# Optimization experiments

Measured on AMD Instinct MI355X. Metric: run time of the kernel, lower is better.

Reference implementation:

```python
import jax, jax.numpy as jnp
import numpy as np

V, H, B, T = 100000, 512, 4096, 524288
EPS = 1e-5

def setup_inputs() -> dict:
    key = jax.random.key(0)
    ks = jax.random.split(key, 8)
    tokens = jax.random.randint(ks[0], (T,), 0, V, dtype=jnp.int32)
    seg_ids = jnp.sort(jax.random.randint(ks[1], (T,), 0, B, dtype=jnp.int32))
    t = jax.random.bernoulli(ks[2], 0.5, (B,)).astype(jnp.float32)
    emb = jax.random.normal(ks[3], (V, H), dtype=jnp.float32) * 0.1
    W1 = jax.random.normal(ks[4], (H, H), dtype=jnp.float32) * (1.0 / np.sqrt(H))
    b1 = jnp.zeros((H,), jnp.float32)
    gamma = jnp.ones((H,), jnp.float32)
    beta = jnp.zeros((H,), jnp.float32)
    w2 = jax.random.normal(ks[5], (H,), dtype=jnp.float32) * (1.0 / np.sqrt(H))
    b2 = jnp.zeros((), jnp.float32)
    return {"tokens": tokens, "seg_ids": seg_ids, "t": t, "emb": emb,
            "W1": W1, "b1": b1, "gamma": gamma, "beta": beta, "w2": w2, "b2": b2}

def reference(tokens, seg_ids, t, emb, W1, b1, gamma, beta, w2, b2):
    nb = t.shape[0]
    # fused gather + segment-mean (bag-of-words), replaces the per-sample loop
    gathered = emb[tokens]  # [T, H]
    sums = jax.ops.segment_sum(gathered, seg_ids, num_segments=nb)  # [B, H]
    counts = jax.ops.segment_sum(jnp.ones((tokens.shape[0],), jnp.float32), seg_ids, num_segments=nb)
    bow = sums / jnp.maximum(counts, 1.0)[:, None]  # [B, H]
    # Linear -> BatchNorm1d (training-mode batch stats, biased var) -> ReLU
    z = bow @ W1.T + b1  # [B, H]
    mu = jnp.mean(z, axis=0)
    var = jnp.mean((z - mu) ** 2, axis=0)
    zn = (z - mu) * jax.lax.rsqrt(var + EPS) * gamma + beta
    h = jax.nn.relu(zn)  # dropout treated as identity (eval mode) for determinism
    logits = h @ w2 + b2  # [B]
    # BCEWithLogitsLoss: mean(softplus(logit) - t*logit), numerically stable
    loss = jnp.mean(jnp.logaddexp(0.0, logits) - t * logits)
    return (loss, logits)
```

## Files before the change

### kernel.cpp

```cpp
#include <hip/hip_runtime.h>
#include <hip/hip_bf16.h>
#include <math.h>

constexpr int NTOK = 524288;
constexpr int NB   = 4096;
constexpr int H    = 512;
constexpr float EPS = 1e-5f;

__global__ __launch_bounds__(128) void k_gather_mean(
    const int* __restrict__ tokens, const int* __restrict__ seg,
    const float* __restrict__ emb, float* __restrict__ bow) {
  const int b = blockIdx.x;
  int lo = 0, hi = NTOK;
  while (lo < hi) { int mid = (lo + hi) >> 1; if (seg[mid] < b) lo = mid + 1; else hi = mid; }
  const int start = lo;
  hi = NTOK;
  while (lo < hi) { int mid = (lo + hi) >> 1; if (seg[mid] < b + 1) lo = mid + 1; else hi = mid; }
  const int end = lo;

  const int tid = threadIdx.x;
  const float4* __restrict__ emb4 = (const float4*)emb;
  float4 acc = make_float4(0.f, 0.f, 0.f, 0.f);

  int i = start;
  for (; i + 4 <= end; i += 4) {
    int t0 = tokens[i], t1 = tokens[i + 1], t2 = tokens[i + 2], t3 = tokens[i + 3];
    float4 v0 = emb4[(size_t)t0 * 128 + tid];
    float4 v1 = emb4[(size_t)t1 * 128 + tid];
    float4 v2 = emb4[(size_t)t2 * 128 + tid];
    float4 v3 = emb4[(size_t)t3 * 128 + tid];
    acc.x += v0.x + v1.x + v2.x + v3.x;
    acc.y += v0.y + v1.y + v2.y + v3.y;
    acc.z += v0.z + v1.z + v2.z + v3.z;
    acc.w += v0.w + v1.w + v2.w + v3.w;
  }
  for (; i < end; ++i) {
    int t0 = tokens[i];
    float4 v0 = emb4[(size_t)t0 * 128 + tid];
    acc.x += v0.x; acc.y += v0.y; acc.z += v0.z; acc.w += v0.w;
  }
  const int cnt = end - start;
  const float s = 1.0f / (float)(cnt > 0 ? cnt : 1);
  acc.x *= s; acc.y *= s; acc.z *= s; acc.w *= s;
  ((float4*)bow)[(size_t)b * 128 + tid] = acc;
}

constexpr int BM = 64, BN = 64, BK = 32;
constexpr int LST = BM + 4;

__global__ __launch_bounds__(256) void k_gemm(
    const float* __restrict__ A, const float* __restrict__ W,
    const float* __restrict__ b1, float* __restrict__ C) {
  __shared__ float As[BK][LST];
  __shared__ float Bs[BK][LST];
  const int tid = threadIdx.x;
  const int tx = tid & 15, ty = tid >> 4;
  const int bm0 = blockIdx.x * BM;
  const int bn0 = blockIdx.y * BN;

  const int lrow = tid >> 3;
  const int lc4  = (tid & 7) * 4;

  float acc[4][4] = {};

  for (int kc = 0; kc < H; kc += BK) {
    float4 a0 = *(const float4*)&A[(size_t)(bm0 + lrow)      * H + kc + lc4];
    float4 a1 = *(const float4*)&A[(size_t)(bm0 + lrow + 32) * H + kc + lc4];
    float4 w0 = *(const float4*)&W[(size_t)(bn0 + lrow)      * H + kc + lc4];
    float4 w1 = *(const float4*)&W[(size_t)(bn0 + lrow + 32) * H + kc + lc4];
    __syncthreads();
    As[lc4 + 0][lrow] = a0.x; As[lc4 + 1][lrow] = a0.y;
    As[lc4 + 2][lrow] = a0.z; As[lc4 + 3][lrow] = a0.w;
    As[lc4 + 0][lrow + 32] = a1.x; As[lc4 + 1][lrow + 32] = a1.y;
    As[lc4 + 2][lrow + 32] = a1.z; As[lc4 + 3][lrow + 32] = a1.w;
    Bs[lc4 + 0][lrow] = w0.x; Bs[lc4 + 1][lrow] = w0.y;
    Bs[lc4 + 2][lrow] = w0.z; Bs[lc4 + 3][lrow] = w0.w;
    Bs[lc4 + 0][lrow + 32] = w1.x; Bs[lc4 + 1][lrow + 32] = w1.y;
    Bs[lc4 + 2][lrow + 32] = w1.z; Bs[lc4 + 3][lrow + 32] = w1.w;
    __syncthreads();
#pragma unroll
    for (int k = 0; k < BK; ++k) {
      float4 av = *(const float4*)&As[k][ty * 4];
      float4 bv = *(const float4*)&Bs[k][tx * 4];
      acc[0][0] += av.x * bv.x; acc[0][1] += av.x * bv.y; acc[0][2] += av.x * bv.z; acc[0][3] += av.x * bv.w;
      acc[1][0] += av.y * bv.x; acc[1][1] += av.y * bv.y; acc[1][2] += av.y * bv.z; acc[1][3] += av.y * bv.w;
      acc[2][0] += av.z * bv.x; acc[2][1] += av.z * bv.y; acc[2][2] += av.z * bv.z; acc[2][3] += av.z * bv.w;
      acc[3][0] += av.w * bv.x; acc[3][1] += av.w * bv.y; acc[3][2] += av.w * bv.z; acc[3][3] += av.w * bv.w;
    }
  }
  const float4 bb = *(const float4*)&b1[bn0 + tx * 4];
#pragma unroll
  for (int i = 0; i < 4; ++i) {
    float4 o;
    o.x = acc[i][0] + bb.x; o.y = acc[i][1] + bb.y;
    o.z = acc[i][2] + bb.z; o.w = acc[i][3] + bb.w;
    *(float4*)&C[(size_t)(bm0 + ty * 4 + i) * H + bn0 + tx * 4] = o;
  }
}

__global__ __launch_bounds__(256) void k_colstats(
    const float* __restrict__ z, float* __restrict__ ps, float* __restrict__ pss) {
  const int blk = blockIdx.x;
  const int c0 = threadIdx.x * 2;
  const int r0 = blk * 64;
  float s0 = 0, s1 = 0, q0 = 0, q1 = 0;
  for (int r = 0; r < 64; ++r) {
    float2 v = *(const float2*)&z[(size_t)(r0 + r) * H + c0];
    s0 += v.x; s1 += v.y;
    q0 += v.x * v.x; q1 += v.y * v.y;
  }
  ps[blk * H + c0] = s0; ps[blk * H + c0 + 1] = s1;
  pss[blk * H + c0] = q0; pss[blk * H + c0 + 1] = q1;
}

__global__ __launch_bounds__(512) void k_finalize(
    const float* __restrict__ ps, const float* __restrict__ pss,
    const float* __restrict__ gamma, const float* __restrict__ beta,
    float* __restrict__ scale, float* __restrict__ shift) {
  const int c = threadIdx.x;
  float s = 0, q = 0;
  for (int i = 0; i < 64; ++i) { s += ps[i * H + c]; q += pss[i * H + c]; }
  const float mu = s * (1.0f / NB);
  const float var = q * (1.0f / NB) - mu * mu;
  const float rstd = rsqrtf(var + EPS);
  const float sc = rstd * gamma[c];
  scale[c] = sc;
  shift[c] = beta[c] - mu * sc;
}

__global__ __launch_bounds__(256) void k_bn_dot(
    const float* __restrict__ z, const float* __restrict__ scale,
    const float* __restrict__ shift, const float* __restrict__ w2,
    const float* __restrict__ b2, float* __restrict__ out) {
  const int tid = threadIdx.x;
  const int wave = tid >> 6, lane = tid & 63;
  const int b = blockIdx.x * 4 + wave;
  const float4* __restrict__ z4 = (const float4*)(z + (size_t)b * H);
  const float4* __restrict__ sc4 = (const float4*)scale;
  const float4* __restrict__ sh4 = (const float4*)shift;
  const float4* __restrict__ w24 = (const float4*)w2;
  float acc = 0.f;
#pragma unroll
  for (int i = lane; i < 128; i += 64) {
    float4 zv = z4[i], sc = sc4[i], sh = sh4[i], w = w24[i];
    float h0 = fmaxf(zv.x * sc.x + sh.x, 0.f);
    float h1 = fmaxf(zv.y * sc.y + sh.y, 0.f);
    float h2 = fmaxf(zv.z * sc.z + sh.z, 0.f);
    float h3 = fmaxf(zv.w * sc.w + sh.w, 0.f);
    acc += h0 * w.x + h1 * w.y + h2 * w.z + h3 * w.w;
  }
#pragma unroll
  for (int off = 32; off > 0; off >>= 1) acc += __shfl_down(acc, off, 64);
  if (lane == 0) out[1 + b] = acc + b2[0];
}

__global__ __launch_bounds__(256) void k_loss(
    const float* __restrict__ t, float* __restrict__ d_out) {
  const int tid = threadIdx.x;
  float s = 0.f;
  for (int b = tid; b < NB; b += 256) {
    float x = d_out[1 + b];
    float sp = fmaxf(x, 0.f) + log1pf(expf(-fabsf(x)));
    s += sp - t[b] * x;
  }
  __shared__ float red[256];
  red[tid] = s;
  __syncthreads();
  for (int off = 128; off > 0; off >>= 1) {
    if (tid < off) red[tid] += red[tid + off];
    __syncthreads();
  }
  if (tid == 0) d_out[0] = red[0] * (1.0f / NB);
}

extern "C" void kernel_launch(void* const* d_in, const int* in_sizes, int n_in,
                              void* d_out, int out_size, void* d_ws, size_t ws_size,
                              hipStream_t stream) {
  const int*   tokens = (const int*)d_in[0];
  const int*   seg    = (const int*)d_in[1];
  const float* t      = (const float*)d_in[2];
  const float* emb    = (const float*)d_in[3];
  const float* W1     = (const float*)d_in[4];
  const float* b1     = (const float*)d_in[5];
  const float* gamma  = (const float*)d_in[6];
  const float* beta   = (const float*)d_in[7];
  const float* w2     = (const float*)d_in[8];
  const float* b2     = (const float*)d_in[9];
  float* out = (float*)d_out;

  float* ws = (float*)d_ws;
  float* bow   = ws;
  float* z     = bow + (size_t)NB * H;
  float* ps    = z + (size_t)NB * H;
  float* pss   = ps + 64 * H;
  float* scale = pss + 64 * H;
  float* shift = scale + H;

  k_gather_mean<<<NB, 128, 0, stream>>>(tokens, seg, emb, bow);
  dim3 ggrid(NB / BM, H / BN);
  k_gemm<<<ggrid, 256, 0, stream>>>(bow, W1, b1, z);
  k_colstats<<<64, 256, 0, stream>>>(z, ps, pss);
  k_finalize<<<1, 512, 0, stream>>>(ps, pss, gamma, beta, scale, shift);
  k_bn_dot<<<NB / 4, 256, 0, stream>>>(z, scale, shift, w2, b2, out);
  k_loss<<<1, 256, 0, stream>>>(t, out);
}
```

Baseline: 461.4 us.

## Convert embedding table to fp16 each call and gather half-precision rows

```diff
diff --git a/kernel.cpp b/kernel.cpp
--- a/kernel.cpp
+++ b/kernel.cpp
@@ -1,5 +1,6 @@
 #include <hip/hip_runtime.h>
 #include <hip/hip_bf16.h>
+#include <hip/hip_fp16.h>
 #include <math.h>
 
 constexpr int NTOK = 524288;
@@ -7,9 +8,21 @@
 constexpr int H    = 512;
 constexpr float EPS = 1e-5f;
 
-__global__ __launch_bounds__(128) void k_gather_mean(
+struct h4 { __half2 a, b; };
+
+__global__ __launch_bounds__(256) void k_convert(
+    const float* __restrict__ emb, h4* __restrict__ embh) {
+  size_t i = (size_t)blockIdx.x * 256 + threadIdx.x;
+  float4 v = ((const float4*)emb)[i];
+  h4 o;
+  o.a = __floats2half2_rn(v.x, v.y);
+  o.b = __floats2half2_rn(v.z, v.w);
+  embh[i] = o;
+}
+
+__global__ __launch_bounds__(256) void k_gather_mean(
     const int* __restrict__ tokens, const int* __restrict__ seg,
-    const float* __restrict__ emb, float* __restrict__ bow) {
+    const h4* __restrict__ embh, float* __restrict__ bow) {
   const int b = blockIdx.x;
   int lo = 0, hi = NTOK;
   while (lo < hi) { int mid = (lo + hi) >> 1; if (seg[mid] < b) lo = mid + 1; else hi = mid; }
@@ -19,30 +32,43 @@
   const int end = lo;
 
   const int tid = threadIdx.x;
-  const float4* __restrict__ emb4 = (const float4*)emb;
+  const int col = tid & 127;
+  const int g = tid >> 7;
+
   float4 acc = make_float4(0.f, 0.f, 0.f, 0.f);
-
-  int i = start;
-  for (; i + 4 <= end; i += 4) {
-    int t0 = tokens[i], t1 = tokens[i + 1], t2 = tokens[i + 2], t3 = tokens[i + 3];
-    float4 v0 = emb4[(size_t)t0 * 128 + tid];
-    float4 v1 = emb4[(size_t)t1 * 128 + tid];
-    float4 v2 = emb4[(size_t)t2 * 128 + tid];
-    float4 v3 = emb4[(size_t)t3 * 128 + tid];
-    acc.x += v0.x + v1.x + v2.x + v3.x;
-    acc.y += v0.y + v1.y + v2.y + v3.y;
-    acc.z += v0.z + v1.z + v2.z + v3.z;
-    acc.w += v0.w + v1.w + v2.w + v3.w;
-  }
-  for (; i < end; ++i) {
-    int t0 = tokens[i];
-    float4 v0 = emb4[(size_t)t0 * 128 + tid];
-    acc.x += v0.x; acc.y += v0.y; acc.z += v0.z; acc.w += v0.w;
-  }
-  const int cnt = end - start;
-  const float s = 1.0f / (float)(cnt > 0 ? cnt : 1);
-  acc.x *= s; acc.y *= s; acc.z *= s; acc.w *= s;
-  ((float4*)bow)[(size_t)b * 128 + tid] = acc;
+  int i = start + g;
+  for (; i + 6 < end; i += 8) {
+    int t0 = tokens[i], t1 = tokens[i + 2], t2 = tokens[i + 4], t3 = tokens[i + 6];
+    h4 v0 = embh[(size_t)t0 * 128 + col];
+    h4 v1 = embh[(size_t)t1 * 128 + col];
+    h4 v2 = embh[(size_t)t2 * 128 + col];
+    h4 v3 = embh[(size_t)t3 * 128 + col];
+    float2 a0 = __half22float2(v0.a), b0 = __half22float2(v0.b);
+    float2 a1 = __half22float2(v1.a), b1 = __half22float2(v1.b);
+    float2 a2 = __half22float2(v2.a), b2 = __half22float2(v2.b);
+    float2 a3 = __half22float2(v3.a), b3 = __half22float2(v3.b);
+    acc.x += a0.x + a1.x + a2.x + a3.x;
+    acc.y += a0.y + a1.y + a2.y + a3.y;
+    acc.z += b0.x + b1.x + b2.x + b3.x;
+    acc.w += b0.y + b1.y + b2.y + b3.y;
+  }
+  for (; i < end; i += 2) {
+    h4 v0 = embh[(size_t)tokens[i] * 128 + col];
+    float2 a0 = __half22float2(v0.a), b0 = __half22float2(v0.b);
+    acc.x += a0.x; acc.y += a0.y; acc.z += b0.x; acc.w += b0.y;
+  }
+
+  __shared__ float4 part[128];
+  if (g == 1) part[col] = acc;
+  __syncthreads();
+  if (g == 0) {
+    float4 p = part[col];
+    const int cnt = end - start;
+    const float s = 1.0f / (float)(cnt > 0 ? cnt : 1);
+    acc.x = (acc.x + p.x) * s; acc.y = (acc.y + p.y) * s;
+    acc.z = (acc.z + p.z) * s; acc.w = (acc.w + p.w) * s;
+    ((float4*)bow)[(size_t)b * 128 + col] = acc;
+  }
 }
 
 constexpr int BM = 64, BN = 64, BK = 32;
@@ -188,15 +214,17 @@
   const float* b2     = (const float*)d_in[9];
   float* out = (float*)d_out;
 
-  float* ws = (float*)d_ws;
-  float* bow   = ws;
+  char* wsb = (char*)d_ws;
+  h4*    embh  = (h4*)wsb;
+  float* bow   = (float*)(wsb + 102400000);
   float* z     = bow + (size_t)NB * H;
   float* ps    = z + (size_t)NB * H;
   float* pss   = ps + 64 * H;
   float* scale = pss + 64 * H;
   float* shift = scale + H;
 
-  k_gather_mean<<<NB, 128, 0, stream>>>(tokens, seg, emb, bow);
+  k_convert<<<50000, 256, 0, stream>>>(emb, embh);
+  k_gather_mean<<<NB, 256, 0, stream>>>(tokens, seg, embh, bow);
   dim3 ggrid(NB / BM, H / BN);
   k_gemm<<<ggrid, 256, 0, stream>>>(bow, W1, b1, z);
   k_colstats<<<64, 256, 0, stream>>>(z, ps, pss);
```

Measured after the change: 445.9 us. 1.03x faster.
